# Performance work log

Measured on AMD Instinct MI355X. Metric: run time of the kernel, lower is better.

Reference implementation:

```python
import jax, jax.numpy as jnp
import numpy as np

HEADS, DIM_KEY, DIM_VALUE, DIM, N, B = 8, 64, 192, 1536, 2048, 2
SCALE = DIM_KEY ** -0.5


def setup_inputs() -> dict:
    key = jax.random.key(0)
    ks = jax.random.split(key, 8)
    s = 0.02
    return {
        "x": jax.random.normal(ks[0], (B, N, DIM), jnp.float32),
        "Wq": jax.random.normal(ks[1], (DIM, HEADS * DIM_KEY), jnp.float32) * s,
        "Wk": jax.random.normal(ks[2], (DIM, HEADS * DIM_KEY), jnp.float32) * s,
        "Wv": jax.random.normal(ks[3], (DIM, HEADS * DIM_VALUE), jnp.float32) * s,
        "Wo": jax.random.normal(ks[4], (HEADS * DIM_VALUE, DIM), jnp.float32) * s,
        "bo": jnp.zeros((DIM,), jnp.float32),
        "pos_embed": jax.random.normal(ks[5], (HEADS, N, DIM_KEY), jnp.float32) * s,
        "rel_content_bias": jax.random.normal(ks[6], (1, HEADS, 1, DIM_KEY), jnp.float32),
    }


def _split_heads(t, d):
    # [B, N, H*d] -> [B, H, N, d]
    b, n, _ = t.shape
    return t.reshape(b, n, HEADS, d).transpose(0, 2, 1, 3)


def reference(x, Wq, Wk, Wv, Wo, bo, pos_embed, rel_content_bias):
    q = _split_heads(x @ Wq, DIM_KEY) * SCALE          # [B,H,N,dk]
    k = _split_heads(x @ Wk, DIM_KEY)                  # [B,H,N,dk]
    v = _split_heads(x @ Wv, DIM_VALUE)                # [B,H,N,dv]
    q_biased = q + pos_embed[None] + rel_content_bias  # additive biases fused into Q
    logits = jnp.einsum('bhid,bhjd->bhij', q_biased, k)
    attn = jax.nn.softmax(logits, axis=-1)
    out = jnp.einsum('bhij,bhjd->bhid', attn, v)       # [B,H,N,dv]
    out = out.transpose(0, 2, 1, 3).reshape(x.shape[0], x.shape[1], HEADS * DIM_VALUE)
    return out @ Wo + bo
```

## Files before the change

### kernel.cpp

```cpp
#include <hip/hip_runtime.h>

#define BB    2
#define HN    8
#define NSEQ  2048
#define DIMM  1536
#define DKD   64
#define DVD   192
#define QCOLS 512
#define VCOLS 1536

typedef short short8 __attribute__((ext_vector_type(8)));
typedef float f32x4  __attribute__((ext_vector_type(4)));
typedef unsigned short ushortT;

static __device__ inline ushortT f2bf(float f) {
    unsigned u = __builtin_bit_cast(unsigned, f);
    u = (u + 0x7FFFu + ((u >> 16) & 1u)) >> 16;
    return (ushortT)u;
}

static __device__ inline void gl_lds16(const ushortT* g, ushortT* l) {
    __builtin_amdgcn_global_load_lds(
        (const __attribute__((address_space(1))) unsigned int*)g,
        (__attribute__((address_space(3))) unsigned int*)l, 16, 0, 0);
}

#define FENCE_VM0()    asm volatile("s_waitcnt vmcnt(0)" ::: "memory")
#define FENCE_VM12()   asm volatile("s_waitcnt vmcnt(12)" ::: "memory")
#define FENCE_LGKM0()  asm volatile("s_waitcnt lgkmcnt(0)" ::: "memory")
#define FENCE_SOFT()   asm volatile("" ::: "memory")

__global__ __launch_bounds__(256)
void prep_kernel(const float* __restrict__ x,
                 const float* __restrict__ Wq, const float* __restrict__ Wk,
                 const float* __restrict__ Wv, const float* __restrict__ Wo,
                 ushortT* __restrict__ xb, ushortT* __restrict__ wqkv,
                 ushortT* __restrict__ wo_t)
{
    __shared__ ushortT tt[32][33];
    const int b = blockIdx.x, tid = threadIdx.x;

    if (b < 3072) {
        const size_t idx = (size_t)b * 256 + tid;
        const float4* p = (const float4*)x + idx * 2;
        const float4 a = p[0], c = p[1];
        short8 v;
        v[0] = f2bf(a.x); v[1] = f2bf(a.y); v[2] = f2bf(a.z); v[3] = f2bf(a.w);
        v[4] = f2bf(c.x); v[5] = f2bf(c.y); v[6] = f2bf(c.z); v[7] = f2bf(c.w);
        *(short8*)(xb + idx * 8) = v;
        return;
    }

    const float* W; ushortT* Wt; int ncols, t;
    if (b < 3840)      { W = Wq; Wt = wqkv;                          ncols = QCOLS; t = b - 3072; }
    else if (b < 4608) { W = Wk; Wt = wqkv + (size_t)QCOLS * DIMM;   ncols = QCOLS; t = b - 3840; }
    else if (b < 6912) { W = Wv; Wt = wqkv + (size_t)2*QCOLS * DIMM; ncols = VCOLS; t = b - 4608; }
    else               { W = Wo; Wt = wo_t;                          ncols = DIMM;  t = b - 6912; }

    const int nbx = ncols >> 5;
    const int c0 = (t % nbx) * 32, k0 = (t / nbx) * 32;
    const int lx = tid & 31, ly = tid >> 5;
    #pragma unroll
    for (int r = 0; r < 4; r++)
        tt[ly + r * 8][lx] = f2bf(W[(size_t)(k0 + ly + r * 8) * ncols + c0 + lx]);
    __syncthreads();
    #pragma unroll
    for (int r = 0; r < 4; r++)
        Wt[(size_t)(c0 + ly + r * 8) * DIMM + k0 + lx] = tt[lx][ly + r * 8];
}

__global__ __launch_bounds__(256)
void gemm_kernel(const ushortT* __restrict__ A, const ushortT* __restrict__ Bt,
                 const float* __restrict__ bo,
                 const float* __restrict__ pos, const float* __restrict__ rcb,
                 ushortT* __restrict__ q_ws, ushortT* __restrict__ k_ws,
                 ushortT* __restrict__ v_ws, float* __restrict__ Cout, int mode)
{
    __shared__ ushortT As[128 * 64];
    __shared__ ushortT Bs[64 * 64];

    const int tid  = threadIdx.x;
    const int wave = tid >> 6, lane = tid & 63;
    const int quad = lane >> 4, l15 = lane & 15;
    const int m0 = blockIdx.y * 128, n0 = blockIdx.x * 64;

    const int sl_r = lane >> 3;
    const int sl_c = ((lane & 7) ^ sl_r) * 8;

    const ushortT* Ab = A  + (size_t)m0 * DIMM;
    const ushortT* Bb = Bt + (size_t)n0 * DIMM;

    f32x4 acc[2][4];
    #pragma unroll
    for (int i = 0; i < 2; i++)
        #pragma unroll
        for (int j = 0; j < 4; j++) acc[i][j] = (f32x4){0.f, 0.f, 0.f, 0.f};

    for (int k0 = 0; k0 < DIMM; k0 += 64) {
        #pragma unroll
        for (int t = 0; t < 4; t++) {
            const int g = wave * 4 + t;
            gl_lds16(Ab + (size_t)(g * 8 + sl_r) * DIMM + k0 + sl_c, &As[g * 512]);
        }
        #pragma unroll
        for (int t = 0; t < 2; t++) {
            const int g = wave * 2 + t;
            gl_lds16(Bb + (size_t)(g * 8 + sl_r) * DIMM + k0 + sl_c, &Bs[g * 512]);
        }
        __syncthreads();

        short8 af[2][2], bf[4][2];
        #pragma unroll
        for (int i = 0; i < 2; i++) {
            const int r = wave * 32 + i * 16 + l15;
            #pragma unroll
            for (int ks = 0; ks < 2; ks++)
                af[i][ks] = *(const short8*)&As[r * 64 + (((ks * 4 + quad) ^ (l15 & 7)) * 8)];
        }
        #pragma unroll
        for (int j = 0; j < 4; j++) {
            const int r = j * 16 + l15;
            #pragma unroll
            for (int ks = 0; ks < 2; ks++)
                bf[j][ks] = *(const short8*)&Bs[r * 64 + (((ks * 4 + quad) ^ (l15 & 7)) * 8)];
        }

        #pragma unroll
        for (int ks = 0; ks < 2; ks++)
            #pragma unroll
            for (int i = 0; i < 2; i++)
                #pragma unroll
                for (int j = 0; j < 4; j++)
                    acc[i][j] = __builtin_amdgcn_mfma_f32_16x16x32_bf16(af[i][ks], bf[j][ks], acc[i][j], 0, 0, 0);

        __syncthreads();
    }

    #pragma unroll
    for (int i = 0; i < 2; i++) {
        #pragma unroll
        for (int j = 0; j < 4; j++) {
            const int gcol = n0 + j * 16 + l15;
            #pragma unroll
            for (int r = 0; r < 4; r++) {
                const int grow = m0 + wave * 32 + i * 16 + quad * 4 + r;
                const float val = acc[i][j][r];
                if (mode == 1) {
                    Cout[(size_t)grow * DIMM + gcol] = val + bo[gcol];
                } else {
                    const int b = grow >> 11, n = grow & (NSEQ - 1);
                    if (gcol < QCOLS) {
                        const int h = gcol >> 6, d = gcol & 63;
                        q_ws[((size_t)(b * HN + h) * NSEQ + n) * DKD + d] =
                            f2bf(val * 0.125f + pos[((size_t)h * NSEQ + n) * DKD + d] + rcb[h * DKD + d]);
                    } else if (gcol < 2 * QCOLS) {
                        const int c = gcol - QCOLS, h = c >> 6, d = c & 63;
                        k_ws[((size_t)(b * HN + h) * NSEQ + n) * DKD + d] = f2bf(val);
                    } else {
                        const int c = gcol - 2 * QCOLS, h = c / DVD, d = c - h * DVD;
                        const int p = (n & ~31) | (((n & 15) << 1) | ((n >> 4) & 1));
                        v_ws[((size_t)(b * HN + h) * DVD + d) * NSEQ + p] = f2bf(val);
                    }
                }
            }
        }
    }
}

#define PLD2 40
#define SHIFT 20.0f

__global__ __launch_bounds__(128)
void flash_kernel(const ushortT* __restrict__ q_ws, const ushortT* __restrict__ k_ws,
                  const ushortT* __restrict__ v_ws, ushortT* __restrict__ attn)
{
    __shared__ ushortT lds[16384 + 2 * 32 * PLD2];

    const int tid = threadIdx.x;
    const int wave = tid >> 6, lane = tid & 63;
    const int quad = lane >> 4, l15 = lane & 15;

    const int bh = blockIdx.x & 15;
    const int qt = blockIdx.x >> 4;
    const int n0 = qt * 32;
    const int b  = bh >> 3, h = bh & 7;

    const ushortT* kg = k_ws + (size_t)bh * NSEQ * DKD + (size_t)(wave * 1024) * DKD;
    const ushortT* vg = v_ws + (size_t)bh * DVD * NSEQ + wave * 1024;

    ushortT* st = lds + wave * 8192;
    ushortT* Pw = lds + 16384 + wave * (32 * PLD2);

    const int k_r = lane >> 3, k_c = ((lane & 7) ^ (k_r & 7)) * 8;
    const int v_r = lane >> 2;
    const int v_c = ((lane & 3) ^ ((v_r >> 1) & 3)) * 8;

    short8 qf[2][2];
    #pragma unroll
    for (int mt = 0; mt < 2; mt++)
        #pragma unroll
        for (int ks = 0; ks < 2; ks++)
            qf[mt][ks] = *(const short8*)(q_ws + ((size_t)bh * NSEQ + n0 + mt * 16 + l15) * DKD + ks * 32 + quad * 8);

    f32x4 o[2][12];
    #pragma unroll
    for (int mt = 0; mt < 2; mt++)
        #pragma unroll
        for (int nt = 0; nt < 12; nt++) o[mt][nt] = (f32x4){0.f, 0.f, 0.f, 0.f};

    float l_part[2][4];
    #pragma unroll
    for (int mt = 0; mt < 2; mt++)
        #pragma unroll
        for (int i = 0; i < 4; i++) l_part[mt][i] = 0.f;

    for (int kt0 = 0; kt0 < 1024; kt0 += 32) {
        FENCE_LGKM0();

        #pragma unroll
        for (int t = 0; t < 4; t++)
            gl_lds16(kg + (size_t)(kt0 + t * 8 + k_r) * DKD + k_c, st + t * 512);
        #pragma unroll
        for (int u = 0; u < 12; u++)
            gl_lds16(vg + (size_t)(u * 16 + v_r) * NSEQ + kt0 + v_c, st + 2048 + u * 512);

        FENCE_VM12();

        f32x4 s[2][2];
        #pragma unroll
        for (int mt = 0; mt < 2; mt++)
            #pragma unroll
            for (int nt = 0; nt < 2; nt++) s[mt][nt] = (f32x4){0.f, 0.f, 0.f, 0.f};
        #pragma unroll
        for (int ks = 0; ks < 2; ks++)
            #pragma unroll
            for (int nt = 0; nt < 2; nt++) {
                const int key = nt * 16 + l15;
                short8 kf = *(const short8*)&st[key * 64 + (((ks * 4 + quad) ^ (key & 7)) * 8)];
                s[0][nt] = __builtin_amdgcn_mfma_f32_16x16x32_bf16(qf[0][ks], kf, s[0][nt], 0, 0, 0);
                s[1][nt] = __builtin_amdgcn_mfma_f32_16x16x32_bf16(qf[1][ks], kf, s[1][nt], 0, 0, 0);
            }

        #pragma unroll
        for (int mt = 0; mt < 2; mt++)
            #pragma unroll
            for (int i = 0; i < 4; i++) {
                const float p0 = __expf(s[mt][0][i] - SHIFT);
                const float p1 = __expf(s[mt][1][i] - SHIFT);
                l_part[mt][i] += p0 + p1;
                unsigned pk;
                asm("v_cvt_pk_bf16_f32 %0, %1, %2" : "=v"(pk) : "v"(p0), "v"(p1));
                *(unsigned*)&Pw[(mt * 16 + quad * 4 + i) * PLD2 + 2 * l15] = pk;
            }

        FENCE_SOFT();

        short8 a[2];
        #pragma unroll
        for (int mt = 0; mt < 2; mt++)
            a[mt] = *(const short8*)&Pw[(mt * 16 + l15) * PLD2 + quad * 8];

        FENCE_VM0();

        #pragma unroll
        for (int nt2 = 0; nt2 < 12; nt2++) {
            const int d = nt2 * 16 + l15;
            short8 vf = *(const short8*)&st[2048 + d * 32 + ((quad ^ ((l15 >> 1) & 3)) * 8)];
            o[0][nt2] = __builtin_amdgcn_mfma_f32_16x16x32_bf16(a[0], vf, o[0][nt2], 0, 0, 0);
            o[1][nt2] = __builtin_amdgcn_mfma_f32_16x16x32_bf16(a[1], vf, o[1][nt2], 0, 0, 0);
        }
    }

    #pragma unroll
    for (int off = 1; off <= 8; off <<= 1)
        #pragma unroll
        for (int mt = 0; mt < 2; mt++)
            #pragma unroll
            for (int i = 0; i < 4; i++)
                l_part[mt][i] += __shfl_xor(l_part[mt][i], off, 64);

    __syncthreads();
    float* ox = (float*)lds;
    float* lx = (float*)(lds + 16384);
    if (wave == 1) {
        #pragma unroll
        for (int mt = 0; mt < 2; mt++)
            #pragma unroll
            for (int nt2 = 0; nt2 < 12; nt2++)
                #pragma unroll
                for (int i = 0; i < 4; i++)
                    ox[(((mt * 12 + nt2) * 4 + i) * 64) + lane] = o[mt][nt2][i];
        #pragma unroll
        for (int mt = 0; mt < 2; mt++)
            #pragma unroll
            for (int i = 0; i < 4; i++)
                lx[(mt * 4 + i) * 64 + lane] = l_part[mt][i];
    }
    __syncthreads();
    if (wave == 0) {
        float inv[2][4];
        #pragma unroll
        for (int mt = 0; mt < 2; mt++)
            #pragma unroll
            for (int i = 0; i < 4; i++)
                inv[mt][i] = 1.f / (l_part[mt][i] + lx[(mt * 4 + i) * 64 + lane]);
        #pragma unroll
        for (int mt = 0; mt < 2; mt++)
            #pragma unroll
            for (int nt2 = 0; nt2 < 12; nt2++)
                #pragma unroll
                for (int i = 0; i < 4; i++) {
                    const float v = o[mt][nt2][i] + ox[(((mt * 12 + nt2) * 4 + i) * 64) + lane];
                    const int n = n0 + mt * 16 + quad * 4 + i;
                    attn[((size_t)b * NSEQ + n) * DIMM + h * DVD + nt2 * 16 + l15] =
                        f2bf(v * inv[mt][i]);
                }
    }
}

extern "C" void kernel_launch(void* const* d_in, const int* in_sizes, int n_in,
                              void* d_out, int out_size, void* d_ws, size_t ws_size,
                              hipStream_t stream)
{
    const float* x   = (const float*)d_in[0];
    const float* Wq  = (const float*)d_in[1];
    const float* Wk  = (const float*)d_in[2];
    const float* Wv  = (const float*)d_in[3];
    const float* Wo  = (const float*)d_in[4];
    const float* bo  = (const float*)d_in[5];
    const float* pos = (const float*)d_in[6];
    const float* rcb = (const float*)d_in[7];
    float* out = (float*)d_out;

    ushortT* xb    = (ushortT*)d_ws;
    ushortT* wqkv  = xb    + (size_t)4096 * DIMM;
    ushortT* wo_t  = wqkv  + (size_t)(2 * QCOLS + VCOLS) * DIMM;
    ushortT* q_ws  = wo_t  + (size_t)DIMM * DIMM;
    ushortT* k_ws  = q_ws  + (size_t)BB * HN * NSEQ * DKD;
    ushortT* v_ws  = k_ws  + (size_t)BB * HN * NSEQ * DKD;
    ushortT* attnb = v_ws  + (size_t)BB * HN * NSEQ * DVD;

    prep_kernel<<<dim3(9216), dim3(256), 0, stream>>>(x, Wq, Wk, Wv, Wo, xb, wqkv, wo_t);

    gemm_kernel<<<dim3(40, 32), dim3(256), 0, stream>>>(xb, wqkv, bo, pos, rcb,
                                                        q_ws, k_ws, v_ws, nullptr, 0);
    flash_kernel<<<dim3(1024), dim3(128), 0, stream>>>(q_ws, k_ws, v_ws, attnb);
    gemm_kernel<<<dim3(24, 32), dim3(256), 0, stream>>>(attnb, wo_t, bo, pos, rcb,
                                                        q_ws, k_ws, v_ws, out, 1);
}
```

Measured before the change: 260.3 us.

## Load V directly into registers and switch softmax to exp2 with prescaled Q

V tiles are no longer staged through LDS. Each lane now loads its MFMA B-operand fragments straight from global memory, in two batches interleaved with the QK^T MFMAs. This cuts the per-block LDS footprint and removes the LDS read traffic for V, which could allow higher occupancy. Separately, Q is prescaled by log2(e) in the projection epilogue so the kernel can use the hardware exp2 instruction with a rescaled shift. The trade-off is strided, less coalesced global loads for V and more registers to hold twelve V fragments.

```diff
diff --git a/kernel.cpp b/kernel.cpp
--- a/kernel.cpp
+++ b/kernel.cpp
@@ -26,7 +26,7 @@
 }
 
 #define FENCE_VM0()    asm volatile("s_waitcnt vmcnt(0)" ::: "memory")
-#define FENCE_VM12()   asm volatile("s_waitcnt vmcnt(12)" ::: "memory")
+#define FENCE_VM6()    asm volatile("s_waitcnt vmcnt(6)" ::: "memory")
 #define FENCE_LGKM0()  asm volatile("s_waitcnt lgkmcnt(0)" ::: "memory")
 #define FENCE_SOFT()   asm volatile("" ::: "memory")
 
@@ -152,7 +152,8 @@
                     if (gcol < QCOLS) {
                         const int h = gcol >> 6, d = gcol & 63;
                         q_ws[((size_t)(b * HN + h) * NSEQ + n) * DKD + d] =
-                            f2bf(val * 0.125f + pos[((size_t)h * NSEQ + n) * DKD + d] + rcb[h * DKD + d]);
+                            f2bf((val * 0.125f + pos[((size_t)h * NSEQ + n) * DKD + d] + rcb[h * DKD + d])
+                                 * 1.4426950408889634f);
                     } else if (gcol < 2 * QCOLS) {
                         const int c = gcol - QCOLS, h = c >> 6, d = c & 63;
                         k_ws[((size_t)(b * HN + h) * NSEQ + n) * DKD + d] = f2bf(val);
@@ -168,13 +169,13 @@
 }
 
 #define PLD2 40
-#define SHIFT 20.0f
+#define SHIFT2 28.8539008178f
 
 __global__ __launch_bounds__(128)
 void flash_kernel(const ushortT* __restrict__ q_ws, const ushortT* __restrict__ k_ws,
                   const ushortT* __restrict__ v_ws, ushortT* __restrict__ attn)
 {
-    __shared__ ushortT lds[16384 + 2 * 32 * PLD2];
+    __shared__ ushortT lds[13312];
 
     const int tid = threadIdx.x;
     const int wave = tid >> 6, lane = tid & 63;
@@ -188,12 +189,12 @@
     const ushortT* kg = k_ws + (size_t)bh * NSEQ * DKD + (size_t)(wave * 1024) * DKD;
     const ushortT* vg = v_ws + (size_t)bh * DVD * NSEQ + wave * 1024;
 
-    ushortT* st = lds + wave * 8192;
-    ushortT* Pw = lds + 16384 + wave * (32 * PLD2);
+    ushortT* st = lds + wave * 2048;
+    ushortT* Pw = lds + 4096 + wave * (32 * PLD2);
 
     const int k_r = lane >> 3, k_c = ((lane & 7) ^ (k_r & 7)) * 8;
-    const int v_r = lane >> 2;
-    const int v_c = ((lane & 3) ^ ((v_r >> 1) & 3)) * 8;
+
+    const ushortT* vb = vg + (size_t)l15 * NSEQ + quad * 8;
 
     short8 qf[2][2];
     #pragma unroll
@@ -220,11 +221,15 @@
         #pragma unroll
         for (int t = 0; t < 4; t++)
             gl_lds16(kg + (size_t)(kt0 + t * 8 + k_r) * DKD + k_c, st + t * 512);
-        #pragma unroll
-        for (int u = 0; u < 12; u++)
-            gl_lds16(vg + (size_t)(u * 16 + v_r) * NSEQ + kt0 + v_c, st + 2048 + u * 512);
-
-        FENCE_VM12();
+
+        FENCE_SOFT();
+
+        short8 vf[12];
+        #pragma unroll
+        for (int n = 0; n < 6; n++)
+            vf[n] = *(const short8*)(vb + (size_t)(n * 16) * NSEQ + kt0);
+
+        FENCE_VM6();
 
         f32x4 s[2][2];
         #pragma unroll
@@ -242,11 +247,15 @@
             }
 
         #pragma unroll
+        for (int n = 6; n < 12; n++)
+            vf[n] = *(const short8*)(vb + (size_t)(n * 16) * NSEQ + kt0);
+
+        #pragma unroll
         for (int mt = 0; mt < 2; mt++)
             #pragma unroll
             for (int i = 0; i < 4; i++) {
-                const float p0 = __expf(s[mt][0][i] - SHIFT);
-                const float p1 = __expf(s[mt][1][i] - SHIFT);
+                const float p0 = __builtin_amdgcn_exp2f(s[mt][0][i] - SHIFT2);
+                const float p1 = __builtin_amdgcn_exp2f(s[mt][1][i] - SHIFT2);
                 l_part[mt][i] += p0 + p1;
                 unsigned pk;
                 asm("v_cvt_pk_bf16_f32 %0, %1, %2" : "=v"(pk) : "v"(p0), "v"(p1));
@@ -260,14 +269,10 @@
         for (int mt = 0; mt < 2; mt++)
             a[mt] = *(const short8*)&Pw[(mt * 16 + l15) * PLD2 + quad * 8];
 
-        FENCE_VM0();
-
         #pragma unroll
         for (int nt2 = 0; nt2 < 12; nt2++) {
-            const int d = nt2 * 16 + l15;
-            short8 vf = *(const short8*)&st[2048 + d * 32 + ((quad ^ ((l15 >> 1) & 3)) * 8)];
-            o[0][nt2] = __builtin_amdgcn_mfma_f32_16x16x32_bf16(a[0], vf, o[0][nt2], 0, 0, 0);
-            o[1][nt2] = __builtin_amdgcn_mfma_f32_16x16x32_bf16(a[1], vf, o[1][nt2], 0, 0, 0);
+            o[0][nt2] = __builtin_amdgcn_mfma_f32_16x16x32_bf16(a[0], vf[nt2], o[0][nt2], 0, 0, 0);
+            o[1][nt2] = __builtin_amdgcn_mfma_f32_16x16x32_bf16(a[1], vf[nt2], o[1][nt2], 0, 0, 0);
         }
     }
 
@@ -281,7 +286,7 @@
 
     __syncthreads();
     float* ox = (float*)lds;
-    float* lx = (float*)(lds + 16384);
+    float* lx = (float*)(lds + 12288);
     if (wave == 1) {
         #pragma unroll
         for (int mt = 0; mt < 2; mt++)
```

New measurement: 289.0 us. +11.0%, slower.
